# Kernel tuning notes

Hardware: AMD Instinct MI355X
Metric: run time of the kernel (lower is better)

Reference implementation:

```python
import jax, jax.numpy as jnp
import numpy as np

T, B, D, H = 512, 128, 512, 512


def setup_inputs() -> dict:
    key = jax.random.key(0)
    ks = jax.random.split(key, 14)
    s = 0.05
    return {
        "inputs": jax.random.normal(ks[0], (T, B, D), dtype=jnp.float32),
        # gate linears: Linear(D+H, out) -> weight [out, D+H], bias [out]
        "Wf": jax.random.normal(ks[1], (2, D + H), dtype=jnp.float32) * s,
        "bf": jax.random.normal(ks[2], (2,), dtype=jnp.float32) * s,
        "Wi": jax.random.normal(ks[3], (H, D + H), dtype=jnp.float32) * s,
        "bi": jax.random.normal(ks[4], (H,), dtype=jnp.float32) * s,
        "Wu": jax.random.normal(ks[5], (H, D + H), dtype=jnp.float32) * s,
        "bu": jax.random.normal(ks[6], (H,), dtype=jnp.float32) * s,
        "Wo": jax.random.normal(ks[7], (H, D + H), dtype=jnp.float32) * s,
        "bo": jax.random.normal(ks[8], (H,), dtype=jnp.float32) * s,
        # SamplerModule: Linear(2,4) -> Tanh -> Linear(4,2) -> softmax
        "Ws1": jax.random.normal(ks[9], (4, 2), dtype=jnp.float32) * 0.5,
        "bs1": jax.random.normal(ks[10], (4,), dtype=jnp.float32) * 0.5,
        "Ws2": jax.random.normal(ks[11], (2, 4), dtype=jnp.float32) * 0.5,
        "bs2": jax.random.normal(ks[12], (2,), dtype=jnp.float32) * 0.5,
    }


def reference(inputs, Wf, bf, Wi, bi, Wu, bu, Wo, bo, Ws1, bs1, Ws2, bs2):
    Bsz = inputs.shape[1]
    h0 = jnp.zeros((Bsz, H), dtype=inputs.dtype)
    c0 = jnp.zeros((Bsz, H), dtype=inputs.dtype)

    def step(carry, x):
        hx, cx = carry
        combined = jnp.concatenate([x, hx], axis=1)  # [B, D+H]
        f_logits = combined @ Wf.T + bf              # [B, 2]
        hdn = jnp.tanh(f_logits @ Ws1.T + bs1)       # [B, 4]
        f_probs = jax.nn.softmax(hdn @ Ws2.T + bs2, axis=-1)  # [B, 2]
        f = f_probs[:, 0:1]                          # [B, 1] forget gate
        i = jax.nn.sigmoid(combined @ Wi.T + bi)
        g = jnp.tanh(combined @ Wu.T + bu)
        o = jax.nn.sigmoid(combined @ Wo.T + bo)
        cx = f * cx + i * g
        hx = o * jnp.tanh(cx)
        return (hx, cx), hx

    (hx, cx), stacked = jax.lax.scan(step, (h0, c0), inputs)
    return stacked, (hx, cx)
```

## Files before the change

### kernel.cpp

```cpp
#include <hip/hip_runtime.h>
#include <cstdint>

#define TT 512
#define BB 128
#define DD 512
#define HH 512
#define KTOT 1024

typedef short bf16x8 __attribute__((ext_vector_type(8)));
typedef float f32x4 __attribute__((ext_vector_type(4)));
typedef unsigned long long u64t;

__device__ inline unsigned short f2bfs(float f) {
    unsigned int u = __builtin_bit_cast(unsigned int, f);
    u = (u + 0x7FFFu + ((u >> 16) & 1u)) >> 16;
    return (unsigned short)u;
}

__device__ inline float sigf(float x) { return 1.f / (1.f + __expf(-x)); }
__device__ inline float tanhfast(float x) { return 2.f * sigf(2.f * x) - 1.f; }

__device__ inline bf16x8 load8w(const float* p) {
    const float4* p4 = (const float4*)p;
    float4 a = p4[0], b = p4[1];
    bf16x8 r;
    r[0] = (short)f2bfs(a.x); r[1] = (short)f2bfs(a.y);
    r[2] = (short)f2bfs(a.z); r[3] = (short)f2bfs(a.w);
    r[4] = (short)f2bfs(b.x); r[5] = (short)f2bfs(b.y);
    r[6] = (short)f2bfs(b.z); r[7] = (short)f2bfs(b.w);
    return r;
}

__global__ __launch_bounds__(256, 1) void qlstm_kernel(
    const float* __restrict__ X,
    const float* __restrict__ Wf, const float* __restrict__ bfb,
    const float* __restrict__ Wi, const float* __restrict__ bi,
    const float* __restrict__ Wu, const float* __restrict__ bu,
    const float* __restrict__ Wo, const float* __restrict__ bo,
    const float* __restrict__ Ws1, const float* __restrict__ bs1,
    const float* __restrict__ Ws2, const float* __restrict__ bs2,
    float* __restrict__ out,
    unsigned int* __restrict__ flags,
    unsigned short* __restrict__ hbuf)
{
    const int tid  = threadIdx.x;
    const int bid  = blockIdx.x;
    const int rg   = bid & 7;
    const int cg   = bid >> 3;
    const int b0   = rg * 16;
    const int lane = tid & 63;
    const int wv   = tid >> 6;
    const int qd   = lane >> 4;
    const int nn   = lane & 15;

    __shared__ float pcp[4][4][16][17];

    bf16x8 wfr[4][8];
    {
        bf16x8 z8;
        #pragma unroll
        for (int j = 0; j < 8; ++j) z8[j] = 0;
        #pragma unroll
        for (int g = 0; g < 4; ++g) {
            const float* Wg = (g == 0) ? Wi : (g == 1) ? Wu : (g == 2) ? Wo : Wf;
            const size_t row = (g == 3) ? (size_t)nn : (size_t)(cg * 16 + nn);
            const bool valid = (g < 3) || (nn < 2);
            #pragma unroll
            for (int j = 0; j < 8; ++j) {
                const int kk = (j < 4) ? (wv * 4 + j) : (16 + wv * 4 + (j - 4));
                wfr[g][j] = valid ? load8w(Wg + row * KTOT + kk * 32 + qd * 8) : z8;
            }
        }
    }

    const int fm = tid >> 4, fn = tid & 15;
    const int gcol = cg * 16 + fn;
    const float bir = bi[gcol], bur = bu[gcol], bor = bo[gcol];
    const float bfr0 = bfb[0], bfr1 = bfb[1];
    float ws1r[8], bs1r[4], ws2r[8];
    #pragma unroll
    for (int j = 0; j < 8; ++j) ws1r[j] = Ws1[j];
    #pragma unroll
    for (int j = 0; j < 4; ++j) bs1r[j] = bs1[j];
    #pragma unroll
    for (int j = 0; j < 8; ++j) ws2r[j] = Ws2[j];
    const float bs2r0 = bs2[0], bs2r1 = bs2[1];

    f32x4 ac[4];
    #pragma unroll
    for (int g = 0; g < 4; ++g) ac[g] = f32x4{0.f, 0.f, 0.f, 0.f};
    {
        bf16x8 xa[4];
        #pragma unroll
        for (int j = 0; j < 4; ++j)
            xa[j] = load8w(X + (size_t)(b0 + nn) * DD + (wv * 4 + j) * 32 + qd * 8);
        #pragma unroll
        for (int j = 0; j < 4; ++j)
            #pragma unroll
            for (int g = 0; g < 4; ++g)
                ac[g] = __builtin_amdgcn_mfma_f32_16x16x32_bf16(xa[j], wfr[g][j], ac[g], 0, 0, 0);
    }

    float cval = 0.f;
    u64t  fv   = 0;

    for (int t = 0; t < TT; ++t) {
        if (t > 0) {
            const u64t* fl = (const u64t*)&flags[((t - 1) * 8 + rg) * 128];
            while (__ballot(((unsigned int)fv == 0u) |
                            ((unsigned int)(fv >> 32) == 0u)) != 0ull) {
                __builtin_amdgcn_s_sleep(1);
                fv = __hip_atomic_load(&fl[lane],
                       __ATOMIC_RELAXED, __HIP_MEMORY_SCOPE_AGENT);
            }
            asm volatile("" ::: "memory");
            const u64t* hb = (const u64t*)(hbuf + (size_t)((t + 1) & 1) * BB * HH);
            u64t hwv[8];
            #pragma unroll
            for (int j = 0; j < 4; ++j) {
                const u64t* hp = hb + (((b0 + nn) * HH + (wv * 4 + j) * 32 + qd * 8) >> 2);
                hwv[2 * j]     = __hip_atomic_load(hp,
                                   __ATOMIC_RELAXED, __HIP_MEMORY_SCOPE_AGENT);
                hwv[2 * j + 1] = __hip_atomic_load(hp + 1,
                                   __ATOMIC_RELAXED, __HIP_MEMORY_SCOPE_AGENT);
            }
            #pragma unroll
            for (int j = 0; j < 4; ++j) {
                bf16x8 ha;
                ((u64t*)&ha)[0] = hwv[2 * j];
                ((u64t*)&ha)[1] = hwv[2 * j + 1];
                #pragma unroll
                for (int g = 0; g < 4; ++g)
                    ac[g] = __builtin_amdgcn_mfma_f32_16x16x32_bf16(ha, wfr[g][4 + j], ac[g], 0, 0, 0);
            }
        }

        #pragma unroll
        for (int g = 0; g < 4; ++g)
            #pragma unroll
            for (int r = 0; r < 4; ++r)
                pcp[wv][g][qd * 4 + r][nn] = ac[g][r];
        __syncthreads();

        float s0g = 0.f, s1g = 0.f, s2g = 0.f, sl0 = 0.f, sl1 = 0.f;
        #pragma unroll
        for (int w = 0; w < 4; ++w) {
            s0g += pcp[w][0][fm][fn];
            s1g += pcp[w][1][fm][fn];
            s2g += pcp[w][2][fm][fn];
            sl0 += pcp[w][3][fm][0];
            sl1 += pcp[w][3][fm][1];
        }
        const float l0 = bfr0 + sl0;
        const float l1 = bfr1 + sl1;
        const float hd0 = tanhfast(ws1r[0] * l0 + ws1r[1] * l1 + bs1r[0]);
        const float hd1 = tanhfast(ws1r[2] * l0 + ws1r[3] * l1 + bs1r[1]);
        const float hd2 = tanhfast(ws1r[4] * l0 + ws1r[5] * l1 + bs1r[2]);
        const float hd3 = tanhfast(ws1r[6] * l0 + ws1r[7] * l1 + bs1r[3]);
        const float s0 = bs2r0 + ws2r[0]*hd0 + ws2r[1]*hd1 + ws2r[2]*hd2 + ws2r[3]*hd3;
        const float s1 = bs2r1 + ws2r[4]*hd0 + ws2r[5]*hd1 + ws2r[6]*hd2 + ws2r[7]*hd3;
        const float fval = sigf(s0 - s1);

        const float iv = sigf(bir + s0g);
        const float gv = tanhfast(bur + s1g);
        const float ov = sigf(bor + s2g);
        cval = fval * cval + iv * gv;
        const float hv = ov * tanhfast(cval);
        const int b = b0 + fm;

        {
            unsigned int ub = (unsigned int)f2bfs(hv);
            unsigned int ob = __shfl_xor(ub, 1);
            if ((fn & 1) == 0) {
                unsigned int* hp = (unsigned int*)(hbuf
                    + (size_t)(t & 1) * BB * HH + (size_t)b * HH + gcol);
                __hip_atomic_store(hp, ub | (ob << 16),
                                   __ATOMIC_RELAXED, __HIP_MEMORY_SCOPE_AGENT);
            }
        }
        asm volatile("s_waitcnt vmcnt(0)" ::: "memory");
        if (lane == 0)
            __hip_atomic_store(&flags[(t * 8 + rg) * 128 + cg * 4 + wv], 1u,
                               __ATOMIC_RELAXED, __HIP_MEMORY_SCOPE_AGENT);

        out[((size_t)t * BB + b) * HH + gcol] = hv;
        if (t == TT - 1) {
            out[(size_t)TT * BB * HH + (size_t)b * HH + gcol] = hv;
            out[(size_t)TT * BB * HH + (size_t)BB * HH + (size_t)b * HH + gcol] = cval;
        }
        if (t + 1 < TT) {
            #pragma unroll
            for (int g = 0; g < 4; ++g) ac[g] = f32x4{0.f, 0.f, 0.f, 0.f};
            bf16x8 xa[4];
            #pragma unroll
            for (int j = 0; j < 4; ++j)
                xa[j] = load8w(X + ((size_t)(t + 1) * BB + b0 + nn) * DD
                               + (wv * 4 + j) * 32 + qd * 8);
            #pragma unroll
            for (int j = 0; j < 4; ++j)
                #pragma unroll
                for (int g = 0; g < 4; ++g)
                    ac[g] = __builtin_amdgcn_mfma_f32_16x16x32_bf16(xa[j], wfr[g][j], ac[g], 0, 0, 0);
            fv = __hip_atomic_load(
                   &((const u64t*)&flags[(t * 8 + rg) * 128])[lane],
                   __ATOMIC_RELAXED, __HIP_MEMORY_SCOPE_AGENT);
        }
    }
}

extern "C" void kernel_launch(void* const* d_in, const int* in_sizes, int n_in,
                              void* d_out, int out_size, void* d_ws, size_t ws_size,
                              hipStream_t stream) {
    const float* X   = (const float*)d_in[0];
    const float* Wf  = (const float*)d_in[1];
    const float* bfb = (const float*)d_in[2];
    const float* Wi  = (const float*)d_in[3];
    const float* bi  = (const float*)d_in[4];
    const float* Wu  = (const float*)d_in[5];
    const float* bu  = (const float*)d_in[6];
    const float* Wo  = (const float*)d_in[7];
    const float* bo  = (const float*)d_in[8];
    const float* Ws1 = (const float*)d_in[9];
    const float* bs1 = (const float*)d_in[10];
    const float* Ws2 = (const float*)d_in[11];
    const float* bs2 = (const float*)d_in[12];
    float* out = (float*)d_out;

    unsigned int*   flags = (unsigned int*)d_ws;
    unsigned short* hbuf  = (unsigned short*)((char*)d_ws + (size_t)TT * 8 * 128 * 4);

    hipMemsetAsync(d_ws, 0, (size_t)TT * 8 * 128 * 4, stream);
    qlstm_kernel<<<dim3(256), dim3(256), 0, stream>>>(
        X, Wf, bfb, Wi, bi, Wu, bu, Wo, bo, Ws1, bs1, Ws2, bs2, out, flags, hbuf);
}
```

Baseline: 1.980 ms.

## Replace per-step flag barrier with step-tagged hidden-state words

Drops the separate flag array and its store-wait-then-flag handshake. Each bf16 hidden value is now packed with a 16-bit step tag into a 32-bit word, and consumers poll the data words directly, re-reading only the chunks whose tag does not match yet. This removes one round trip of global memory latency per timestep on the critical recurrence path. In exchange the hidden buffer is twice as large and every poll reads more data.

```diff
diff --git a/kernel.cpp b/kernel.cpp
--- a/kernel.cpp
+++ b/kernel.cpp
@@ -40,8 +40,7 @@
     const float* __restrict__ Ws1, const float* __restrict__ bs1,
     const float* __restrict__ Ws2, const float* __restrict__ bs2,
     float* __restrict__ out,
-    unsigned int* __restrict__ flags,
-    unsigned short* __restrict__ hbuf)
+    unsigned int* __restrict__ hbuf)
 {
     const int tid  = threadIdx.x;
     const int bid  = blockIdx.x;
@@ -102,33 +101,43 @@
     }
 
     float cval = 0.f;
-    u64t  fv   = 0;
+    u64t  hw[16];
+    unsigned int pend = 0;
 
     for (int t = 0; t < TT; ++t) {
         if (t > 0) {
-            const u64t* fl = (const u64t*)&flags[((t - 1) * 8 + rg) * 128];
-            while (__ballot(((unsigned int)fv == 0u) |
-                            ((unsigned int)(fv >> 32) == 0u)) != 0ull) {
+            const u64t pat = ((u64t)(unsigned int)t << 16)
+                           | ((u64t)(unsigned int)t << 48);
+            const unsigned int* hb = hbuf + (size_t)((t - 1) & 1) * BB * HH;
+            for (;;) {
+                unsigned int np = 0;
+                #pragma unroll
+                for (int i = 0; i < 16; ++i)
+                    if ((pend >> i) & 1)
+                        if ((hw[i] & 0xFFFF0000FFFF0000ull) != pat) np |= 1u << i;
+                pend = np;
+                if (__ballot(np != 0u) == 0ull) break;
                 __builtin_amdgcn_s_sleep(1);
-                fv = __hip_atomic_load(&fl[lane],
-                       __ATOMIC_RELAXED, __HIP_MEMORY_SCOPE_AGENT);
-            }
-            asm volatile("" ::: "memory");
-            const u64t* hb = (const u64t*)(hbuf + (size_t)((t + 1) & 1) * BB * HH);
-            u64t hwv[8];
-            #pragma unroll
-            for (int j = 0; j < 4; ++j) {
-                const u64t* hp = hb + (((b0 + nn) * HH + (wv * 4 + j) * 32 + qd * 8) >> 2);
-                hwv[2 * j]     = __hip_atomic_load(hp,
-                                   __ATOMIC_RELAXED, __HIP_MEMORY_SCOPE_AGENT);
-                hwv[2 * j + 1] = __hip_atomic_load(hp + 1,
-                                   __ATOMIC_RELAXED, __HIP_MEMORY_SCOPE_AGENT);
+                #pragma unroll
+                for (int j = 0; j < 4; ++j) {
+                    const u64t* bp = (const u64t*)(hb + (size_t)(b0 + nn) * HH
+                                                   + (wv * 4 + j) * 32 + qd * 8);
+                    #pragma unroll
+                    for (int k = 0; k < 4; ++k)
+                        if ((np >> (j * 4 + k)) & 1)
+                            hw[j * 4 + k] = __hip_atomic_load(bp + k,
+                                __ATOMIC_RELAXED, __HIP_MEMORY_SCOPE_AGENT);
+                }
             }
             #pragma unroll
             for (int j = 0; j < 4; ++j) {
                 bf16x8 ha;
-                ((u64t*)&ha)[0] = hwv[2 * j];
-                ((u64t*)&ha)[1] = hwv[2 * j + 1];
+                #pragma unroll
+                for (int e = 0; e < 8; ++e) {
+                    const u64t w = hw[j * 4 + (e >> 1)];
+                    ha[e] = (short)((e & 1) ? (unsigned int)(w >> 32)
+                                            : (unsigned int)w);
+                }
                 #pragma unroll
                 for (int g = 0; g < 4; ++g)
                     ac[g] = __builtin_amdgcn_mfma_f32_16x16x32_bf16(ha, wfr[g][4 + j], ac[g], 0, 0, 0);
@@ -169,19 +178,16 @@
         const int b = b0 + fm;
 
         {
-            unsigned int ub = (unsigned int)f2bfs(hv);
-            unsigned int ob = __shfl_xor(ub, 1);
+            unsigned int myw = ((unsigned int)(t + 1) << 16)
+                             | (unsigned int)f2bfs(hv);
+            unsigned int nbw = __shfl_xor(myw, 1);
             if ((fn & 1) == 0) {
-                unsigned int* hp = (unsigned int*)(hbuf
-                    + (size_t)(t & 1) * BB * HH + (size_t)b * HH + gcol);
-                __hip_atomic_store(hp, ub | (ob << 16),
-                                   __ATOMIC_RELAXED, __HIP_MEMORY_SCOPE_AGENT);
-            }
-        }
-        asm volatile("s_waitcnt vmcnt(0)" ::: "memory");
-        if (lane == 0)
-            __hip_atomic_store(&flags[(t * 8 + rg) * 128 + cg * 4 + wv], 1u,
-                               __ATOMIC_RELAXED, __HIP_MEMORY_SCOPE_AGENT);
+                u64t pw = (u64t)myw | ((u64t)nbw << 32);
+                __hip_atomic_store(
+                    (u64t*)(hbuf + (size_t)(t & 1) * BB * HH + (size_t)b * HH + gcol),
+                    pw, __ATOMIC_RELAXED, __HIP_MEMORY_SCOPE_AGENT);
+            }
+        }
 
         out[((size_t)t * BB + b) * HH + gcol] = hv;
         if (t == TT - 1) {
@@ -201,9 +207,17 @@
                 #pragma unroll
                 for (int g = 0; g < 4; ++g)
                     ac[g] = __builtin_amdgcn_mfma_f32_16x16x32_bf16(xa[j], wfr[g][j], ac[g], 0, 0, 0);
-            fv = __hip_atomic_load(
-                   &((const u64t*)&flags[(t * 8 + rg) * 128])[lane],
-                   __ATOMIC_RELAXED, __HIP_MEMORY_SCOPE_AGENT);
+            const unsigned int* hb = hbuf + (size_t)(t & 1) * BB * HH;
+            #pragma unroll
+            for (int j = 0; j < 4; ++j) {
+                const u64t* bp = (const u64t*)(hb + (size_t)(b0 + nn) * HH
+                                               + (wv * 4 + j) * 32 + qd * 8);
+                #pragma unroll
+                for (int k = 0; k < 4; ++k)
+                    hw[j * 4 + k] = __hip_atomic_load(bp + k,
+                        __ATOMIC_RELAXED, __HIP_MEMORY_SCOPE_AGENT);
+            }
+            pend = 0xFFFFu;
         }
     }
 }
@@ -226,10 +240,8 @@
     const float* bs2 = (const float*)d_in[12];
     float* out = (float*)d_out;
 
-    unsigned int*   flags = (unsigned int*)d_ws;
-    unsigned short* hbuf  = (unsigned short*)((char*)d_ws + (size_t)TT * 8 * 128 * 4);
-
-    hipMemsetAsync(d_ws, 0, (size_t)TT * 8 * 128 * 4, stream);
+    unsigned int* hbuf = (unsigned int*)d_ws;
+    hipMemsetAsync(d_ws, 0, (size_t)2 * BB * HH * sizeof(unsigned int), stream);
     qlstm_kernel<<<dim3(256), dim3(256), 0, stream>>>(
-        X, Wf, bfb, Wi, bi, Wu, bu, Wo, bo, Ws1, bs1, Ws2, bs2, out, flags, hbuf);
-}
+        X, Wf, bfb, Wi, bi, Wu, bu, Wo, bo, Ws1, bs1, Ws2, bs2, out, hbuf);
+}
```

Result: slower. 3.061 ms (+54.6%).
